# Performance work log

Measured on AMD Instinct MI355X. Metric: run time of the kernel, lower is better.

## Reference

```python
import jax, jax.numpy as jnp
import numpy as np

NEG_INF = -1e9

def setup_inputs() -> dict:
    key = jax.random.key(0)
    ks = jax.random.split(key, 6)
    B, M, RNN, H, D = 64, 1024, 1024, 512, 2048
    return {
        "h": jax.random.normal(ks[0], (B, RNN), dtype=jnp.float32),
        "att_feats": jax.random.normal(ks[1], (B, M, D), dtype=jnp.float32),
        "att_mask": jax.random.randint(ks[2], (B, M), 0, 2, dtype=jnp.int32),
        "p_att_feats": jax.random.normal(ks[3], (B, M, H), dtype=jnp.float32),
        "W_ah": jax.random.normal(ks[4], (H, RNN), dtype=jnp.float32) * (1.0 / np.sqrt(RNN)),
        "w_alpha": jax.random.normal(ks[5], (H,), dtype=jnp.float32) * (1.0 / np.sqrt(H)),
    }

def reference(h, att_feats, att_mask, p_att_feats, W_ah, w_alpha):
    # Wah(h): [B, H]
    wah = h @ W_ah.T
    # additive attention energies: tanh(Wah(h)[:, None, :] + p_att_feats) -> [B, M, H]
    e = jnp.tanh(wah[:, None, :] + p_att_feats)
    # project to scalar per region: [B, M]
    logits = jnp.einsum("bmh,h->bm", e, w_alpha)
    logits = jnp.where(att_mask == 0, NEG_INF, logits)
    alpha = jax.nn.softmax(logits, axis=-1)
    # weighted sum of region features: [B, D]
    att = jnp.einsum("bm,bmd->bd", alpha, att_feats)
    return att
```

## Files before the change

### kernel.cpp

```cpp
#include <hip/hip_runtime.h>
#include <math.h>

#define B   64
#define M   1024
#define RNN 1024
#define H   512
#define D   2048

#define NCHUNK 16
#define CROWS  (M / NCHUNK)
#define RPW    (CROWS / 4)

__device__ __forceinline__ float fast_tanh(float x) {
    float ax = fabsf(x);
    float t  = __expf(-2.0f * ax);
    float r  = (1.0f - t) * __builtin_amdgcn_rcpf(1.0f + t);
    return copysignf(r, x);
}

__global__ __launch_bounds__(256) void k_wah(const float* __restrict__ h,
                                             const float* __restrict__ W,
                                             float* __restrict__ wah) {
    const int tid = threadIdx.x, lane = tid & 63, w = tid >> 6;
    const int bt = blockIdx.y * 16;
    const int j0 = blockIdx.x * 8 + w * 2;

    __shared__ float s_h[16 * RNN];
    const float4* h4  = (const float4*)(h + (size_t)bt * RNN);
    float4*       sh4 = (float4*)s_h;
#pragma unroll
    for (int k = 0; k < 16; ++k)
        sh4[tid + k * 256] = h4[tid + k * 256];

    const float4* Wa = (const float4*)(W + (size_t)j0 * RNN);
    const float4* Wb = (const float4*)(W + (size_t)(j0 + 1) * RNN);
    float4 wa[4], wb[4];
#pragma unroll
    for (int k = 0; k < 4; ++k) { wa[k] = Wa[lane + 64 * k]; wb[k] = Wb[lane + 64 * k]; }
    __syncthreads();

    for (int b = 0; b < 16; ++b) {
        float d0 = 0.0f, d1 = 0.0f;
#pragma unroll
        for (int k = 0; k < 4; ++k) {
            float4 hv = sh4[b * 256 + lane + 64 * k];
            d0 += hv.x * wa[k].x + hv.y * wa[k].y + hv.z * wa[k].z + hv.w * wa[k].w;
            d1 += hv.x * wb[k].x + hv.y * wb[k].y + hv.z * wb[k].z + hv.w * wb[k].w;
        }
#pragma unroll
        for (int off = 32; off > 0; off >>= 1) {
            d0 += __shfl_xor(d0, off);
            d1 += __shfl_xor(d1, off);
        }
        if (lane == 0)
            *(float2*)(wah + (size_t)(bt + b) * H + j0) = make_float2(d0, d1);
    }
}

__global__ __launch_bounds__(256, 4) void k_fused(const float* __restrict__ wah,
                                                  const float* __restrict__ p_att,
                                                  const int* __restrict__ mask,
                                                  const float* __restrict__ w_alpha,
                                                  const float* __restrict__ feats,
                                                  float* __restrict__ partial,
                                                  float* __restrict__ zpart) {
    const int b   = blockIdx.x;
    const int c   = blockIdx.y;
    const int tid = threadIdx.x;
    const int lane = tid & 63;
    const int w    = tid >> 6;

    __shared__ float s_acc[4][D];
    __shared__ float s_z[4];

    const float4* wh4 = (const float4*)(wah + (size_t)b * H);
    const float4* wa4 = (const float4*)w_alpha;
    float4 wh0 = wh4[lane], wh1 = wh4[lane + 64];
    float4 wa0 = wa4[lane], wa1 = wa4[lane + 64];

    const int     m0   = c * CROWS;
    const int*    mrow = mask + (size_t)b * M + m0;
    const float4* pb4  = (const float4*)(p_att + ((size_t)b * M + m0) * H);
    const float4* fb4  = (const float4*)(feats + ((size_t)b * M + m0) * D);

    float4 acc[8];
#pragma unroll
    for (int j = 0; j < 8; ++j) acc[j] = make_float4(0.f, 0.f, 0.f, 0.f);
    float zsum = 0.0f;

    for (int r = w * RPW; r < w * RPW + RPW; ++r) {
        if (mrow[r] == 0) continue;
        const float4* pr = pb4 + (size_t)r * (H / 4);
        const float4* fr = fb4 + (size_t)r * (D / 4) + lane;
        float4 p0 = pr[lane], p1 = pr[lane + 64];
        float4 f0 = fr[0],   f1 = fr[64],  f2 = fr[128], f3 = fr[192];
        float4 f4 = fr[256], f5 = fr[320], f6 = fr[384], f7 = fr[448];

        float s = fast_tanh(p0.x + wh0.x) * wa0.x
                + fast_tanh(p0.y + wh0.y) * wa0.y
                + fast_tanh(p0.z + wh0.z) * wa0.z
                + fast_tanh(p0.w + wh0.w) * wa0.w
                + fast_tanh(p1.x + wh1.x) * wa1.x
                + fast_tanh(p1.y + wh1.y) * wa1.y
                + fast_tanh(p1.z + wh1.z) * wa1.z
                + fast_tanh(p1.w + wh1.w) * wa1.w;
#pragma unroll
        for (int off = 32; off > 0; off >>= 1)
            s += __shfl_xor(s, off);
        float e = __expf(s);
        zsum += e;

        acc[0].x += e * f0.x; acc[0].y += e * f0.y; acc[0].z += e * f0.z; acc[0].w += e * f0.w;
        acc[1].x += e * f1.x; acc[1].y += e * f1.y; acc[1].z += e * f1.z; acc[1].w += e * f1.w;
        acc[2].x += e * f2.x; acc[2].y += e * f2.y; acc[2].z += e * f2.z; acc[2].w += e * f2.w;
        acc[3].x += e * f3.x; acc[3].y += e * f3.y; acc[3].z += e * f3.z; acc[3].w += e * f3.w;
        acc[4].x += e * f4.x; acc[4].y += e * f4.y; acc[4].z += e * f4.z; acc[4].w += e * f4.w;
        acc[5].x += e * f5.x; acc[5].y += e * f5.y; acc[5].z += e * f5.z; acc[5].w += e * f5.w;
        acc[6].x += e * f6.x; acc[6].y += e * f6.y; acc[6].z += e * f6.z; acc[6].w += e * f6.w;
        acc[7].x += e * f7.x; acc[7].y += e * f7.y; acc[7].z += e * f7.z; acc[7].w += e * f7.w;
    }

#pragma unroll
    for (int j = 0; j < 8; ++j)
        *(float4*)&s_acc[w][j * 256 + lane * 4] = acc[j];
    if (lane == 0) s_z[w] = zsum;
    __syncthreads();

    if (tid == 0)
        zpart[(size_t)c * B + b] = (s_z[0] + s_z[1]) + (s_z[2] + s_z[3]);

    float* pout = partial + ((size_t)c * B + b) * D;
#pragma unroll
    for (int k = 0; k < 8; ++k) {
        int d = k * 256 + tid;
        pout[d] = (s_acc[0][d] + s_acc[1][d]) + (s_acc[2][d] + s_acc[3][d]);
    }
}

__global__ __launch_bounds__(256) void k_reduce(const float* __restrict__ partial,
                                                const float* __restrict__ zpart,
                                                float* __restrict__ out) {
    int i4 = blockIdx.x * 256 + threadIdx.x;
    int b  = i4 >> 9;
    float Z = 0.0f;
#pragma unroll
    for (int c = 0; c < NCHUNK; ++c)
        Z += zpart[c * B + b];
    const float4* p4 = (const float4*)partial;
    float4 s = p4[i4];
#pragma unroll
    for (int c = 1; c < NCHUNK; ++c) {
        float4 v = p4[(size_t)c * (B * D / 4) + i4];
        s.x += v.x; s.y += v.y; s.z += v.z; s.w += v.w;
    }
    float inv = 1.0f / Z;
    float4 r = {s.x * inv, s.y * inv, s.z * inv, s.w * inv};
    ((float4*)out)[i4] = r;
}

extern "C" void kernel_launch(void* const* d_in, const int* in_sizes, int n_in,
                              void* d_out, int out_size, void* d_ws, size_t ws_size,
                              hipStream_t stream) {
    const float* h       = (const float*)d_in[0];
    const float* feats   = (const float*)d_in[1];
    const int*   mask    = (const int*)d_in[2];
    const float* p_att   = (const float*)d_in[3];
    const float* W_ah    = (const float*)d_in[4];
    const float* w_alpha = (const float*)d_in[5];
    float* out = (float*)d_out;

    float* ws      = (float*)d_ws;
    float* wah     = ws;
    float* zpart   = wah + B * H;
    float* partial = zpart + NCHUNK * B;

    k_wah   <<<dim3(H / 8, B / 16), 256, 0, stream>>>(h, W_ah, wah);
    k_fused <<<dim3(B, NCHUNK), 256, 0, stream>>>(wah, p_att, mask, w_alpha, feats,
                                                  partial, zpart);
    k_reduce<<<dim3(B * D / 1024), 256, 0, stream>>>(partial, zpart, out);
}
```

Measured before the change: 76.69 us.

## Split fused attention into a score phase and a compacted feature-accumulation phase

The fused kernel now runs in two phases. First each warp computes exp-scores for its masked-in rows from vectorised mask loads and a fully unrolled loop, writing them to shared memory. The nonzero rows are then compacted with a ballot into an index list, and the feature accumulation loop is balanced across warps over only the active rows. The chunk count doubles to raise parallelism, and the reduce kernel is resized to match, at the cost of more partial buffers to write and sum.

```diff
diff --git a/kernel.cpp b/kernel.cpp
--- a/kernel.cpp
+++ b/kernel.cpp
@@ -7,7 +7,7 @@
 #define H   512
 #define D   2048
 
-#define NCHUNK 16
+#define NCHUNK 32
 #define CROWS  (M / NCHUNK)
 #define RPW    (CROWS / 4)
 
@@ -70,46 +70,78 @@
     const int lane = tid & 63;
     const int w    = tid >> 6;
 
-    __shared__ float s_acc[4][D];
-    __shared__ float s_z[4];
+    __shared__ float          s_acc[4][D];
+    __shared__ float          s_w[CROWS];
+    __shared__ float          s_z[4];
+    __shared__ unsigned short s_idx[CROWS];
+    __shared__ float          s_val[CROWS];
+    __shared__ int            s_cnt;
 
     const float4* wh4 = (const float4*)(wah + (size_t)b * H);
     const float4* wa4 = (const float4*)w_alpha;
     float4 wh0 = wh4[lane], wh1 = wh4[lane + 64];
     float4 wa0 = wa4[lane], wa1 = wa4[lane + 64];
 
-    const int     m0   = c * CROWS;
-    const int*    mrow = mask + (size_t)b * M + m0;
-    const float4* pb4  = (const float4*)(p_att + ((size_t)b * M + m0) * H);
-    const float4* fb4  = (const float4*)(feats + ((size_t)b * M + m0) * D);
+    const int m0 = c * CROWS;
+
+    if (lane < RPW) s_w[w * RPW + lane] = 0.0f;
+
+    const int* mrow = mask + (size_t)b * M + m0 + w * RPW;
+    int mk[RPW];
+    *(int4*)&mk[0] = *(const int4*)(mrow);
+    *(int4*)&mk[4] = *(const int4*)(mrow + 4);
+
+    const float4* pb4 = (const float4*)(p_att + ((size_t)b * M + m0 + w * RPW) * H);
+    float zsum = 0.0f;
+#pragma unroll
+    for (int r = 0; r < RPW; ++r) {
+        if (mk[r] != 0) {
+            float4 p0 = pb4[(size_t)r * (H / 4) + lane];
+            float4 p1 = pb4[(size_t)r * (H / 4) + 64 + lane];
+            float s = fast_tanh(p0.x + wh0.x) * wa0.x
+                    + fast_tanh(p0.y + wh0.y) * wa0.y
+                    + fast_tanh(p0.z + wh0.z) * wa0.z
+                    + fast_tanh(p0.w + wh0.w) * wa0.w
+                    + fast_tanh(p1.x + wh1.x) * wa1.x
+                    + fast_tanh(p1.y + wh1.y) * wa1.y
+                    + fast_tanh(p1.z + wh1.z) * wa1.z
+                    + fast_tanh(p1.w + wh1.w) * wa1.w;
+#pragma unroll
+            for (int off = 32; off > 0; off >>= 1)
+                s += __shfl_xor(s, off);
+            float e = __expf(s);
+            if (lane == 0) s_w[w * RPW + r] = e;
+            zsum += e;
+        }
+    }
+    if (lane == 0) s_z[w] = zsum;
+    __syncthreads();
+
+    if (tid == 0)
+        zpart[(size_t)c * B + b] = (s_z[0] + s_z[1]) + (s_z[2] + s_z[3]);
+
+    if (tid < CROWS) {
+        float a = s_w[tid];
+        bool pred = (a != 0.0f);
+        unsigned long long bal = __ballot(pred);
+        int pos = __popcll(bal & ((1ull << lane) - 1ull));
+        if (pred) { s_idx[pos] = (unsigned short)tid; s_val[pos] = a; }
+        if (lane == 0) s_cnt = __popcll(bal);
+    }
+    __syncthreads();
+    const int n = s_cnt;
 
     float4 acc[8];
 #pragma unroll
     for (int j = 0; j < 8; ++j) acc[j] = make_float4(0.f, 0.f, 0.f, 0.f);
-    float zsum = 0.0f;
-
-    for (int r = w * RPW; r < w * RPW + RPW; ++r) {
-        if (mrow[r] == 0) continue;
-        const float4* pr = pb4 + (size_t)r * (H / 4);
-        const float4* fr = fb4 + (size_t)r * (D / 4) + lane;
-        float4 p0 = pr[lane], p1 = pr[lane + 64];
+
+    const float* fbase = feats + ((size_t)b * M + m0) * D;
+    for (int i = w; i < n; i += 4) {
+        int   ridx = s_idx[i];
+        float e    = s_val[i];
+        const float4* fr = (const float4*)(fbase + (size_t)ridx * D) + lane;
         float4 f0 = fr[0],   f1 = fr[64],  f2 = fr[128], f3 = fr[192];
         float4 f4 = fr[256], f5 = fr[320], f6 = fr[384], f7 = fr[448];
-
-        float s = fast_tanh(p0.x + wh0.x) * wa0.x
-                + fast_tanh(p0.y + wh0.y) * wa0.y
-                + fast_tanh(p0.z + wh0.z) * wa0.z
-                + fast_tanh(p0.w + wh0.w) * wa0.w
-                + fast_tanh(p1.x + wh1.x) * wa1.x
-                + fast_tanh(p1.y + wh1.y) * wa1.y
-                + fast_tanh(p1.z + wh1.z) * wa1.z
-                + fast_tanh(p1.w + wh1.w) * wa1.w;
-#pragma unroll
-        for (int off = 32; off > 0; off >>= 1)
-            s += __shfl_xor(s, off);
-        float e = __expf(s);
-        zsum += e;
-
         acc[0].x += e * f0.x; acc[0].y += e * f0.y; acc[0].z += e * f0.z; acc[0].w += e * f0.w;
         acc[1].x += e * f1.x; acc[1].y += e * f1.y; acc[1].z += e * f1.z; acc[1].w += e * f1.w;
         acc[2].x += e * f2.x; acc[2].y += e * f2.y; acc[2].z += e * f2.z; acc[2].w += e * f2.w;
@@ -123,11 +155,7 @@
 #pragma unroll
     for (int j = 0; j < 8; ++j)
         *(float4*)&s_acc[w][j * 256 + lane * 4] = acc[j];
-    if (lane == 0) s_z[w] = zsum;
-    __syncthreads();
-
-    if (tid == 0)
-        zpart[(size_t)c * B + b] = (s_z[0] + s_z[1]) + (s_z[2] + s_z[3]);
+    __syncthreads();
 
     float* pout = partial + ((size_t)c * B + b) * D;
 #pragma unroll
@@ -137,10 +165,10 @@
     }
 }
 
-__global__ __launch_bounds__(256) void k_reduce(const float* __restrict__ partial,
+__global__ __launch_bounds__(128) void k_reduce(const float* __restrict__ partial,
                                                 const float* __restrict__ zpart,
                                                 float* __restrict__ out) {
-    int i4 = blockIdx.x * 256 + threadIdx.x;
+    int i4 = blockIdx.x * 128 + threadIdx.x;
     int b  = i4 >> 9;
     float Z = 0.0f;
 #pragma unroll
@@ -177,5 +205,5 @@
     k_wah   <<<dim3(H / 8, B / 16), 256, 0, stream>>>(h, W_ah, wah);
     k_fused <<<dim3(B, NCHUNK), 256, 0, stream>>>(wah, p_att, mask, w_alpha, feats,
                                                   partial, zpart);
-    k_reduce<<<dim3(B * D / 1024), 256, 0, stream>>>(partial, zpart, out);
-}
+    k_reduce<<<dim3(B * D / 512), 128, 0, stream>>>(partial, zpart, out);
+}
```

Result: slower. 81.88 us (+6.8%).
